# Performance work log

Measured on AMD Instinct MI355X. Metric: run time of the kernel, lower is better.

The kernel has to match this reference:

```python
import jax, jax.numpy as jnp
import numpy as np

B = 50000        # mini-batch nodes
NB, M, D = 4, 256, 32   # branches, codebook size, per-branch dim
C = NB * D       # in_channels = out_channels = 128
E = 1000000      # edges per block (intra and cross)
N_GLOBAL = 100000


def setup_inputs() -> dict:
    key = jax.random.key(0)
    ks = jax.random.split(key, 16)
    return {
        "X_B": jax.random.normal(ks[0], (B, C), dtype=jnp.float32),
        "edge_src_bb": jax.random.randint(ks[1], (E,), 0, B),
        "edge_dst_bb": jax.random.randint(ks[2], (E,), 0, B),
        "edge_w_bb": jax.random.uniform(ks[3], (E,), dtype=jnp.float32),
        "edge_src_bm": jax.random.randint(ks[4], (E,), 0, N_GLOBAL),
        "edge_dst_bm": jax.random.randint(ks[5], (E,), 0, B),
        "edge_w_bm": jax.random.uniform(ks[6], (E,), dtype=jnp.float32),
        "c_indices": jax.random.randint(ks[7], (N_GLOBAL,), 0, M),
        "warm_up_rate": jnp.ones((1,), dtype=jnp.float32),
        "codebook": jax.random.normal(ks[8], (NB, M, D), dtype=jnp.float32),
        "vq_grad": jax.random.normal(ks[9], (NB, M, D), dtype=jnp.float32) * 0.01,
        "W_conv": jax.random.normal(ks[10], (NB, D, D), dtype=jnp.float32) / np.sqrt(D),
        "b_conv": jax.random.normal(ks[11], (NB, D), dtype=jnp.float32) * 0.01,
        "W_fc": jax.random.normal(ks[12], (C, C), dtype=jnp.float32) / np.sqrt(C),
        "b_fc": jax.random.normal(ks[13], (C,), dtype=jnp.float32) * 0.01,
    }


def reference(X_B, edge_src_bb, edge_dst_bb, edge_w_bb, edge_src_bm, edge_dst_bm,
              edge_w_bm, c_indices, warm_up_rate, codebook, vq_grad,
              W_conv, b_conv, W_fc, b_fc):
    wr = warm_up_rate[0]
    # split features into NB branches: [NB, B, D]
    Xb = X_B.reshape(B, NB, D).transpose(1, 0, 2)
    # X_input = cat([X_B, codebook * warm_up_rate]) per branch -> [NB, B+M, D]
    X_in = jnp.concatenate([Xb, codebook * wr], axis=1)
    # GCNConv (normalize=False): linear transform then edge-weighted aggregation
    h = jnp.einsum('nbd,nde->nbe', X_in, W_conv)
    # mapper: remap out-of-batch endpoints of cross edges to codeword rows
    src_bm = B + c_indices[edge_src_bm]          # [E] indices into codeword rows
    out = jnp.zeros_like(h)
    # A_BB block: intra-batch message passing
    out = out.at[:, edge_dst_bb].add(edge_w_bb[None, :, None] * h[:, edge_src_bb])
    # A_BM block: batch nodes receive from codewords (quantized neighbors)
    out = out.at[:, edge_dst_bm].add(edge_w_bm[None, :, None] * h[:, src_bm])
    # A_MB block: codeword rows receive from batch nodes (for info_backward)
    out = out.at[:, src_bm].add(edge_w_bm[None, :, None] * h[:, edge_dst_bm])
    out = out + b_conv[:, None, :]
    # info_backward routes approximated gradient through codeword outputs
    info_backward = jnp.sum(out[:, B:] * vq_grad) * wr
    # concat branch outputs for batch nodes, second fc, skip connection
    Xcat = out[:, :B].transpose(1, 0, 2).reshape(B, C)
    Y = Xcat @ W_fc + b_fc + X_B
    return (Y, info_backward)
```

## Files before the change

kernel.cpp:

```cpp
#include <hip/hip_runtime.h>
#include <hip/hip_bf16.h>

#define BN    50000
#define NBR   4
#define MM    256
#define DD    32
#define CC    128
#define EE    1000000
#define ROWS  (BN + MM)
#define NEDGE (2 * EE)
#define SCAN_BLOCKS 49

template <int ISBF> struct IO;

template <> struct IO<0> {
    static __device__ float ld(const void* p, long i) { return ((const float*)p)[i]; }
    static __device__ float2 ld2(const void* p, long i) {
        const float* f = (const float*)p + i;
        return make_float2(f[0], f[1]);
    }
    static __device__ void st(void* p, long i, float v) { ((float*)p)[i] = v; }
    static __device__ void st2(void* p, long i, float2 v) {
        float* f = (float*)p + i; f[0] = v.x; f[1] = v.y;
    }
};

template <> struct IO<1> {
    static __device__ float b2f(unsigned short u) {
        return __uint_as_float(((unsigned)u) << 16);
    }
    static __device__ unsigned short f2b(float f) {
        unsigned x = __float_as_uint(f);
        unsigned r = x + 0x7fffu + ((x >> 16) & 1u);
        return (unsigned short)(r >> 16);
    }
    static __device__ float ld(const void* p, long i) {
        return b2f(((const unsigned short*)p)[i]);
    }
    static __device__ float2 ld2(const void* p, long i) {
        unsigned v = *(const unsigned*)((const unsigned short*)p + i);
        return make_float2(b2f((unsigned short)(v & 0xffffu)),
                           b2f((unsigned short)(v >> 16)));
    }
    static __device__ void st(void* p, long i, float v) {
        ((unsigned short*)p)[i] = f2b(v);
    }
    static __device__ void st2(void* p, long i, float2 v) {
        unsigned o = ((unsigned)f2b(v.x)) | (((unsigned)f2b(v.y)) << 16);
        *(unsigned*)((unsigned short*)p + i) = o;
    }
};

template <int ISBF> struct HIO;
template <> struct HIO<0> {
    static __device__ float2 ld(const float* h, long row, int l) {
        return *(const float2*)(h + row * CC + 2 * l);
    }
    static __device__ void st(float* h, long row, int l, float2 v) {
        *(float2*)(h + row * CC + 2 * l) = v;
    }
};
template <> struct HIO<1> {
    static __device__ float2 ld(const float* h, long row, int l) {
        unsigned u = ((const unsigned*)h)[row * (CC / 2) + l];
        return make_float2(IO<1>::b2f((unsigned short)(u & 0xffffu)),
                           IO<1>::b2f((unsigned short)(u >> 16)));
    }
    static __device__ void st(float* h, long row, int l, float2 v) {
        unsigned o = ((unsigned)IO<1>::f2b(v.x)) | (((unsigned)IO<1>::f2b(v.y)) << 16);
        ((unsigned*)h)[row * (CC / 2) + l] = o;
    }
};

static __device__ inline void unpack8(int4 v, float* f) {
    unsigned a = (unsigned)v.x, b = (unsigned)v.y, c = (unsigned)v.z, d = (unsigned)v.w;
    f[0] = IO<1>::b2f((unsigned short)(a & 0xffffu)); f[1] = IO<1>::b2f((unsigned short)(a >> 16));
    f[2] = IO<1>::b2f((unsigned short)(b & 0xffffu)); f[3] = IO<1>::b2f((unsigned short)(b >> 16));
    f[4] = IO<1>::b2f((unsigned short)(c & 0xffffu)); f[5] = IO<1>::b2f((unsigned short)(c >> 16));
    f[6] = IO<1>::b2f((unsigned short)(d & 0xffffu)); f[7] = IO<1>::b2f((unsigned short)(d >> 16));
}
static __device__ inline void fma8(float* acc, float w, int4 v) {
    float f[8]; unpack8(v, f);
#pragma unroll
    for (int k = 0; k < 8; k++) acc[k] += w * f[k];
}
static __device__ inline float dot8(const float* hi, int4 v) {
    float f[8]; unpack8(v, f);
    float s = 0.f;
#pragma unroll
    for (int k = 0; k < 8; k++) s += hi[k] * f[k];
    return s;
}

__global__ void kDetect(const void* warm, int* flag) {
    flag[0] = (((const unsigned short*)warm)[0] == 0x3F80u) ? 1 : 0;
}

template <int ISBF>
__device__ void kA_body(const void* X_B, const void* codebook, const void* W_conv,
                        const void* warm, float* __restrict__ hout,
                        float* __restrict__ hcw, float* sW, float* sX) {
    int tid = threadIdx.x;
    int w = tid >> 6, l = tid & 63;
    for (int k = tid; k < NBR * DD * DD; k += 256)
        sW[k] = IO<ISBF>::ld(W_conv, k);
    int r = blockIdx.x * 4 + w;
    int c0 = 2 * l, n = c0 >> 5, e = c0 & 31;
    float2 x2;
    if (r < BN) {
        x2 = IO<ISBF>::ld2(X_B, (long)r * CC + c0);
    } else {
        int m = r - BN;
        float wr = IO<ISBF>::ld(warm, 0);
        x2 = IO<ISBF>::ld2(codebook, (long)n * MM * DD + m * DD + e);
        x2.x *= wr; x2.y *= wr;
    }
    sX[w * CC + c0] = x2.x;
    sX[w * CC + c0 + 1] = x2.y;
    __syncthreads();
    float2 acc = make_float2(0.f, 0.f);
#pragma unroll
    for (int d = 0; d < DD; d++) {
        float xv = sX[w * CC + n * DD + d];
        float2 wv = *(const float2*)&sW[n * DD * DD + d * DD + e];
        acc.x += xv * wv.x;
        acc.y += xv * wv.y;
    }
    if (r < BN) HIO<ISBF>::st(hout, r, l, acc);
    else        HIO<ISBF>::st(hcw, r - BN, l, acc);
}
__global__ __launch_bounds__(256) void kA(const int* flag, const void* X_B,
                                          const void* codebook, const void* W_conv,
                                          const void* warm, float* hout, float* hcw) {
    __shared__ float sW[NBR * DD * DD];
    __shared__ float sX[4 * CC];
    if (*flag) kA_body<1>(X_B, codebook, W_conv, warm, hout, hcw, sW, sX);
    else       kA_body<0>(X_B, codebook, W_conv, warm, hout, hcw, sW, sX);
}

__global__ void kHist(const int* __restrict__ edst_bb, const int* __restrict__ edst_bm,
                      int* __restrict__ counts) {
    long stride = (long)gridDim.x * blockDim.x;
    for (long i = (long)blockIdx.x * blockDim.x + threadIdx.x; i < NEDGE; i += stride) {
        int dst = (i < EE) ? edst_bb[i] : edst_bm[i - EE];
        atomicAdd(&counts[dst], 1);
    }
}

__global__ __launch_bounds__(1024) void kScan1(const int* __restrict__ counts,
                                               int* __restrict__ offsets,
                                               int* __restrict__ tileSum) {
    __shared__ int s[1024];
    int tid = threadIdx.x;
    int i = blockIdx.x * 1024 + tid;
    int v = (i < BN) ? counts[i] : 0;
    s[tid] = v;
    __syncthreads();
    for (int off = 1; off < 1024; off <<= 1) {
        int x = (tid >= off) ? s[tid - off] : 0;
        __syncthreads();
        s[tid] += x;
        __syncthreads();
    }
    if (i < BN) offsets[i] = s[tid] - v;
    if (tid == 1023) tileSum[blockIdx.x] = s[tid];
}
__global__ void kScan2(int* tileSum) {
    int run = 0;
    for (int t = 0; t < SCAN_BLOCKS; t++) {
        int v = tileSum[t];
        tileSum[t] = run;
        run += v;
    }
}
__global__ __launch_bounds__(1024) void kScan3(int* __restrict__ offsets,
                                               const int* __restrict__ tileSum,
                                               int* __restrict__ cursor) {
    int i = blockIdx.x * 1024 + threadIdx.x;
    if (i < BN) {
        int o = offsets[i] + tileSum[blockIdx.x];
        offsets[i] = o;
        cursor[i] = o;
    }
}

template <int ISBF>
__device__ void kFill_body(const int* esrc_bb, const int* edst_bb, const void* ew_bb,
                           const int* esrc_bm, const int* edst_bm, const void* ew_bm,
                           const int* c_idx, int* cursor, int2* entries) {
    long stride = (long)gridDim.x * blockDim.x;
    for (long i = (long)blockIdx.x * blockDim.x + threadIdx.x; i < NEDGE; i += stride) {
        int src, dst; float w;
        if (i < EE) {
            src = esrc_bb[i]; dst = edst_bb[i]; w = IO<ISBF>::ld(ew_bb, i);
        } else {
            long j = i - EE;
            src = BN + c_idx[esrc_bm[j]]; dst = edst_bm[j]; w = IO<ISBF>::ld(ew_bm, j);
        }
        int pos = atomicAdd(&cursor[dst], 1);
        entries[pos] = make_int2(src, __float_as_int(w));
    }
}
__global__ void kFill(const int* flag, const int* esrc_bb, const int* edst_bb,
                      const void* ew_bb, const int* esrc_bm, const int* edst_bm,
                      const void* ew_bm, const int* c_idx, int* cursor, int2* entries) {
    if (*flag) kFill_body<1>(esrc_bb, edst_bb, ew_bb, esrc_bm, edst_bm, ew_bm, c_idx, cursor, entries);
    else       kFill_body<0>(esrc_bb, edst_bb, ew_bb, esrc_bm, edst_bm, ew_bm, c_idx, cursor, entries);
}

__device__ void kG_body_bf(const unsigned short* __restrict__ hbatch,
                           const unsigned short* __restrict__ hcw,
                           const int2* __restrict__ entries,
                           const int* __restrict__ offsets, const int* __restrict__ counts,
                           const void* b_conv, const void* vq_grad, void* t,
                           float* __restrict__ infoP, int4* sCW) {
    int tid = threadIdx.x;
    const int4* cwsrc = (const int4*)hcw;
    for (int k = tid; k < MM * CC * 2 / 16; k += 1024) sCW[k] = cwsrc[k];
    __syncthreads();
    const char* sB = (const char*)sCW;

    int w = tid >> 6, l = tid & 63;
    int i = blockIdx.x * 16 + w;
    int g = l >> 4;
    int q = l & 15;
    int c0 = q * 8;
    int n = c0 >> 5, e0 = c0 & 31;
    int start = __builtin_amdgcn_readfirstlane(offsets[i]);
    int deg   = __builtin_amdgcn_readfirstlane(counts[i]);
    const int2* ep = entries + start;
    const unsigned short* gb = (const unsigned short*)vq_grad + (long)n * MM * DD + e0;

    float hi[8];
    unpack8(*(const int4*)(hbatch + (long)i * CC + c0), hi);
    float acc[8] = {0.f, 0.f, 0.f, 0.f, 0.f, 0.f, 0.f, 0.f};
    float info = 0.f;

    int j = 0;
    for (; j + 32 <= deg; j += 32) {
        int2 ev[8];
#pragma unroll
        for (int u = 0; u < 8; u++) ev[u] = ep[j + 4 * u + g];
#pragma unroll
        for (int u = 0; u < 8; u++) {
            float wj = __int_as_float(ev[u].y);
            int4 hv;
            if (ev[u].x < BN) {
                hv = *(const int4*)(hbatch + (long)ev[u].x * CC + c0);
            } else {
                hv = *(const int4*)(sB + (((long)(ev[u].x - BN)) << 8) + (q << 4));
                int4 gv = *(const int4*)(gb + (long)(ev[u].x - BN) * DD);
                info += wj * dot8(hi, gv);
            }
            fma8(acc, wj, hv);
        }
    }
    for (; j < deg; j += 4) {
        int idx = j + g;
        int2 ev = ep[idx < deg ? idx : j];
        float wj = (idx < deg) ? __int_as_float(ev.y) : 0.f;
        int4 hv;
        if (ev.x < BN) {
            hv = *(const int4*)(hbatch + (long)ev.x * CC + c0);
        } else {
            hv = *(const int4*)(sB + (((long)(ev.x - BN)) << 8) + (q << 4));
            if (wj != 0.f) {
                int4 gv = *(const int4*)(gb + (long)(ev.x - BN) * DD);
                info += wj * dot8(hi, gv);
            }
        }
        fma8(acc, wj, hv);
    }
#pragma unroll
    for (int k = 0; k < 8; k++) {
        acc[k] += __shfl_xor(acc[k], 16);
        acc[k] += __shfl_xor(acc[k], 32);
    }
    for (int off = 32; off; off >>= 1) info += __shfl_xor(info, off);
    if (l == 0) infoP[i] = info;
    if (g == 0) {
        float bc[8];
        unpack8(*(const int4*)((const unsigned short*)b_conv + n * DD + e0), bc);
        unsigned o[4];
#pragma unroll
        for (int d = 0; d < 4; d++)
            o[d] = ((unsigned)IO<1>::f2b(acc[2 * d] + bc[2 * d])) |
                   (((unsigned)IO<1>::f2b(acc[2 * d + 1] + bc[2 * d + 1])) << 16);
        *(int4*)((unsigned short*)t + (long)i * CC + c0) = make_int4(o[0], o[1], o[2], o[3]);
    }
}

__device__ void kG_body_f32(const float* __restrict__ hbatch, const float* __restrict__ hcw,
                            const int2* __restrict__ entries,
                            const int* __restrict__ offsets, const int* __restrict__ counts,
                            const void* b_conv, const void* vq_grad, void* t,
                            float* __restrict__ infoP) {
    int tid = threadIdx.x;
    int w = tid >> 6, l = tid & 63;
    int i = blockIdx.x * 16 + w;
    int c0 = 2 * l, n = c0 >> 5, e = c0 & 31;
    int start = __builtin_amdgcn_readfirstlane(offsets[i]);
    int deg   = __builtin_amdgcn_readfirstlane(counts[i]);
    const int2* ep = entries + start;
    float2 hi = HIO<0>::ld(hbatch, i, l);
    long gbase = (long)n * MM * DD + e;
    float2 acc = make_float2(0.f, 0.f);
    float info = 0.f;
    for (int j = 0; j < deg; j++) {
        int2 ev = ep[j];
        float wj = __int_as_float(ev.y);
        const float* src = (ev.x < BN) ? (hbatch + (long)ev.x * CC)
                                       : (hcw + (long)(ev.x - BN) * CC);
        float2 hv = *(const float2*)(src + c0);
        acc.x += wj * hv.x;
        acc.y += wj * hv.y;
        if (ev.x >= BN) {
            float2 gv = IO<0>::ld2(vq_grad, gbase + (long)(ev.x - BN) * DD);
            info += wj * (hi.x * gv.x + hi.y * gv.y);
        }
    }
    float2 b2 = IO<0>::ld2(b_conv, n * DD + e);
    IO<0>::st2(t, (long)i * CC + c0, make_float2(acc.x + b2.x, acc.y + b2.y));
    for (int off = 32; off; off >>= 1) info += __shfl_xor(info, off);
    if (l == 0) infoP[i] = info;
}
__global__ __launch_bounds__(1024, 8) void kGather(const int* flag, const float* hout,
                                                   const float* hcw, const int2* entries,
                                                   const int* offsets, const int* counts,
                                                   const void* b_conv, const void* vq_grad,
                                                   void* t, float* infoP) {
    __shared__ int4 sCW[MM * CC * 2 / 16];
    if (*flag) kG_body_bf((const unsigned short*)hout, (const unsigned short*)hcw,
                          entries, offsets, counts, b_conv, vq_grad, t, infoP, sCW);
    else       kG_body_f32(hout, hcw, entries, offsets, counts, b_conv, vq_grad, t, infoP);
}

__global__ __launch_bounds__(1024) void kRed(const float* __restrict__ infoP, float* ibAcc) {
    __shared__ float s[1024];
    int tid = threadIdx.x;
    int i = blockIdx.x * 1024 + tid;
    s[tid] = (i < BN) ? infoP[i] : 0.f;
    __syncthreads();
    for (int st = 512; st; st >>= 1) {
        if (tid < st) s[tid] += s[tid + st];
        __syncthreads();
    }
    if (tid == 0) atomicAdd(ibAcc, s[0]);
}

template <int ISBF>
__device__ void kFC_body(const void* t, const void* W_fc, const void* b_fc,
                         const void* X_B, void* Y, float* sT, float* sW) {
    int tid = threadIdx.x;
    int w = tid >> 6, l = tid & 63;
    int c0 = 2 * l;
    int r0 = blockIdx.x * 32;
    for (int k = tid; k < 32 * CC / 2; k += 512) {
        int row = k >> 6, c = (k & 63) * 2;
        float2 v = make_float2(0.f, 0.f);
        if (r0 + row < BN) v = IO<ISBF>::ld2(t, (long)(r0 + row) * CC + c);
        sT[row * CC + c] = v.x;
        sT[row * CC + c + 1] = v.y;
    }
    float2 y[4];
#pragma unroll
    for (int rr = 0; rr < 4; rr++) y[rr] = make_float2(0.f, 0.f);
    for (int ch = 0; ch < 4; ch++) {
        __syncthreads();
        for (int k = tid; k < 32 * CC / 2; k += 512) {
            int cc = k >> 6, c = (k & 63) * 2;
            float2 v = IO<ISBF>::ld2(W_fc, (long)(ch * 32 + cc) * CC + c);
            sW[cc * CC + c] = v.x;
            sW[cc * CC + c + 1] = v.y;
        }
        __syncthreads();
#pragma unroll 8
        for (int cc = 0; cc < 32; cc++) {
            float2 wv = *(const float2*)&sW[cc * CC + c0];
#pragma unroll
            for (int rr = 0; rr < 4; rr++) {
                float tv = sT[(w * 4 + rr) * CC + ch * 32 + cc];
                y[rr].x += tv * wv.x;
                y[rr].y += tv * wv.y;
            }
        }
    }
    float2 bf = IO<ISBF>::ld2(b_fc, c0);
#pragma unroll
    for (int rr = 0; rr < 4; rr++) {
        int r = r0 + w * 4 + rr;
        if (r < BN) {
            float2 xb = IO<ISBF>::ld2(X_B, (long)r * CC + c0);
            IO<ISBF>::st2(Y, (long)r * CC + c0,
                          make_float2(y[rr].x + bf.x + xb.x, y[rr].y + bf.y + xb.y));
        }
    }
}
__global__ __launch_bounds__(512) void kFC(const int* flag, const void* t, const void* W_fc,
                                           const void* b_fc, const void* X_B, void* Y) {
    __shared__ float sT[32 * CC];
    __shared__ float sW[32 * CC];
    if (*flag) kFC_body<1>(t, W_fc, b_fc, X_B, Y, sT, sW);
    else       kFC_body<0>(t, W_fc, b_fc, X_B, Y, sT, sW);
}

template <int ISBF>
__device__ void kF_body(const void* b_conv, const void* vq_grad, const void* warm,
                        const float* ibAcc, void* out, float* sred) {
    int tid = threadIdx.x;
    float a = 0.f;
    for (int idx = tid; idx < NBR * MM * DD; idx += 256) {
        int nn = idx >> 13, dd = idx & 31;
        a += IO<ISBF>::ld(b_conv, nn * DD + dd) * IO<ISBF>::ld(vq_grad, idx);
    }
    sred[tid] = a;
    __syncthreads();
    for (int s = 128; s; s >>= 1) {
        if (tid < s) sred[tid] += sred[tid + s];
        __syncthreads();
    }
    if (tid == 0) {
        float wr = IO<ISBF>::ld(warm, 0);
        IO<ISBF>::st(out, (long)BN * CC, wr * (ibAcc[0] + sred[0]));
    }
}
__global__ __launch_bounds__(256) void kFinal(const int* flag, const void* b_conv,
                                              const void* vq_grad, const void* warm,
                                              const float* ibAcc, void* out) {
    __shared__ float sred[256];
    if (*flag) kF_body<1>(b_conv, vq_grad, warm, ibAcc, out, sred);
    else       kF_body<0>(b_conv, vq_grad, warm, ibAcc, out, sred);
}

extern "C" void kernel_launch(void* const* d_in, const int* in_sizes, int n_in,
                              void* d_out, int out_size, void* d_ws, size_t ws_size,
                              hipStream_t stream) {
    (void)in_sizes; (void)n_in; (void)out_size;
    const void* X_B      = d_in[0];
    const int*  esrc_bb  = (const int*)d_in[1];
    const int*  edst_bb  = (const int*)d_in[2];
    const void* ew_bb    = d_in[3];
    const int*  esrc_bm  = (const int*)d_in[4];
    const int*  edst_bm  = (const int*)d_in[5];
    const void* ew_bm    = d_in[6];
    const int*  c_idx    = (const int*)d_in[7];
    const void* warm     = d_in[8];
    const void* codebook = d_in[9];
    const void* vq_grad  = d_in[10];
    const void* W_conv   = d_in[11];
    const void* b_conv   = d_in[12];
    const void* W_fc     = d_in[13];
    const void* b_fc     = d_in[14];

    char* ws = (char*)d_ws;
    float* hcw     = (float*)ws;  ws += (size_t)MM * CC * 4;
    float* tbuf    = (float*)ws;  ws += (size_t)BN * CC * 4;
    int2*  entries = (int2*)ws;   ws += (size_t)NEDGE * 8;
    int*   counts  = (int*)ws;    ws += (size_t)BN * 4;
    int*   offsets = (int*)ws;    ws += (size_t)BN * 4;
    int*   cursor  = (int*)ws;    ws += (size_t)BN * 4;
    float* infoP   = (float*)ws;  ws += (size_t)BN * 4;
    int*   tileSum = (int*)ws;    ws += 64 * 4;
    float* ibAcc   = (float*)ws;  ws += 16;
    int*   flag    = (int*)ws;    ws += 16;
    if ((size_t)(ws - (char*)d_ws) > ws_size) return;

    float* hout = (float*)d_out;

    hipMemsetAsync(counts, 0, (size_t)BN * 4, stream);
    hipMemsetAsync(ibAcc, 0, 4, stream);
    kDetect<<<1, 1, 0, stream>>>(warm, flag);
    kA<<<ROWS / 4, 256, 0, stream>>>(flag, X_B, codebook, W_conv, warm, hout, hcw);
    kHist<<<1024, 256, 0, stream>>>(edst_bb, edst_bm, counts);
    kScan1<<<SCAN_BLOCKS, 1024, 0, stream>>>(counts, offsets, tileSum);
    kScan2<<<1, 1, 0, stream>>>(tileSum);
    kScan3<<<SCAN_BLOCKS, 1024, 0, stream>>>(offsets, tileSum, cursor);
    kFill<<<1024, 256, 0, stream>>>(flag, esrc_bb, edst_bb, ew_bb, esrc_bm, edst_bm,
                                    ew_bm, c_idx, cursor, entries);
    kGather<<<BN / 16, 1024, 0, stream>>>(flag, hout, hcw, entries, offsets, counts,
                                          b_conv, vq_grad, tbuf, infoP);
    kRed<<<SCAN_BLOCKS, 1024, 0, stream>>>(infoP, ibAcc);
    kFC<<<(BN + 31) / 32, 512, 0, stream>>>(flag, tbuf, W_fc, b_fc, X_B, d_out);
    kFinal<<<1, 256, 0, stream>>>(flag, b_conv, vq_grad, warm, ibAcc, d_out);
}
```

Before: 659.1 us.

## Use persistent grid-stride gather and drop shared-memory codebook staging

The gather kernel becomes persistent: 2048 blocks of 256 threads, with each wavefront striding over destination rows, instead of one 1024-thread block per 16 rows. The per-block copy of the codeword features into shared memory, and the barrier after it, are removed. Codeword rows are now read from global memory and are expected to stay in cache. The main loop and the tail loop are merged into one clamped, masked loop. This cuts the repeated 64KB LDS staging and the launch overhead, but codeword reads now go through L2/L1 instead of LDS.

```diff
diff --git a/kernel.cpp b/kernel.cpp
--- a/kernel.cpp
+++ b/kernel.cpp
@@ -213,80 +213,70 @@
                            const int2* __restrict__ entries,
                            const int* __restrict__ offsets, const int* __restrict__ counts,
                            const void* b_conv, const void* vq_grad, void* t,
-                           float* __restrict__ infoP, int4* sCW) {
-    int tid = threadIdx.x;
-    const int4* cwsrc = (const int4*)hcw;
-    for (int k = tid; k < MM * CC * 2 / 16; k += 1024) sCW[k] = cwsrc[k];
-    __syncthreads();
-    const char* sB = (const char*)sCW;
-
-    int w = tid >> 6, l = tid & 63;
-    int i = blockIdx.x * 16 + w;
+                           float* __restrict__ infoP) {
+    int tid = threadIdx.x;
+    int l = tid & 63;
     int g = l >> 4;
     int q = l & 15;
     int c0 = q * 8;
     int n = c0 >> 5, e0 = c0 & 31;
-    int start = __builtin_amdgcn_readfirstlane(offsets[i]);
-    int deg   = __builtin_amdgcn_readfirstlane(counts[i]);
-    const int2* ep = entries + start;
     const unsigned short* gb = (const unsigned short*)vq_grad + (long)n * MM * DD + e0;
 
-    float hi[8];
-    unpack8(*(const int4*)(hbatch + (long)i * CC + c0), hi);
-    float acc[8] = {0.f, 0.f, 0.f, 0.f, 0.f, 0.f, 0.f, 0.f};
-    float info = 0.f;
-
-    int j = 0;
-    for (; j + 32 <= deg; j += 32) {
-        int2 ev[8];
-#pragma unroll
-        for (int u = 0; u < 8; u++) ev[u] = ep[j + 4 * u + g];
-#pragma unroll
-        for (int u = 0; u < 8; u++) {
-            float wj = __int_as_float(ev[u].y);
-            int4 hv;
-            if (ev[u].x < BN) {
-                hv = *(const int4*)(hbatch + (long)ev[u].x * CC + c0);
-            } else {
-                hv = *(const int4*)(sB + (((long)(ev[u].x - BN)) << 8) + (q << 4));
-                int4 gv = *(const int4*)(gb + (long)(ev[u].x - BN) * DD);
-                info += wj * dot8(hi, gv);
+    int wid = (int)((blockIdx.x * blockDim.x + tid) >> 6);
+    int nw  = (int)((gridDim.x * blockDim.x) >> 6);
+
+    for (int i = wid; i < BN; i += nw) {
+        int start = __builtin_amdgcn_readfirstlane(offsets[i]);
+        int deg   = __builtin_amdgcn_readfirstlane(counts[i]);
+        const int2* ep = entries + start;
+
+        float hi[8];
+        unpack8(*(const int4*)(hbatch + (long)i * CC + c0), hi);
+        float acc[8] = {0.f, 0.f, 0.f, 0.f, 0.f, 0.f, 0.f, 0.f};
+        float info = 0.f;
+
+        for (int j = 0; j < deg; j += 32) {
+            int2 ev[8];
+            float wj[8];
+#pragma unroll
+            for (int u = 0; u < 8; u++) {
+                int idx = j + 4 * u + g;
+                int cl = idx < deg ? idx : deg - 1;
+                ev[u] = ep[cl];
+                wj[u] = (idx < deg) ? __int_as_float(ev[u].y) : 0.f;
             }
-            fma8(acc, wj, hv);
-        }
-    }
-    for (; j < deg; j += 4) {
-        int idx = j + g;
-        int2 ev = ep[idx < deg ? idx : j];
-        float wj = (idx < deg) ? __int_as_float(ev.y) : 0.f;
-        int4 hv;
-        if (ev.x < BN) {
-            hv = *(const int4*)(hbatch + (long)ev.x * CC + c0);
-        } else {
-            hv = *(const int4*)(sB + (((long)(ev.x - BN)) << 8) + (q << 4));
-            if (wj != 0.f) {
-                int4 gv = *(const int4*)(gb + (long)(ev.x - BN) * DD);
-                info += wj * dot8(hi, gv);
+#pragma unroll
+            for (int u = 0; u < 8; u++) {
+                int4 hv;
+                if (ev[u].x < BN) {
+                    hv = *(const int4*)(hbatch + (long)ev[u].x * CC + c0);
+                } else {
+                    hv = *(const int4*)(hcw + (long)(ev[u].x - BN) * CC + c0);
+                    if (wj[u] != 0.f) {
+                        int4 gv = *(const int4*)(gb + (long)(ev[u].x - BN) * DD);
+                        info += wj[u] * dot8(hi, gv);
+                    }
+                }
+                fma8(acc, wj[u], hv);
             }
         }
-        fma8(acc, wj, hv);
-    }
-#pragma unroll
-    for (int k = 0; k < 8; k++) {
-        acc[k] += __shfl_xor(acc[k], 16);
-        acc[k] += __shfl_xor(acc[k], 32);
-    }
-    for (int off = 32; off; off >>= 1) info += __shfl_xor(info, off);
-    if (l == 0) infoP[i] = info;
-    if (g == 0) {
-        float bc[8];
-        unpack8(*(const int4*)((const unsigned short*)b_conv + n * DD + e0), bc);
-        unsigned o[4];
-#pragma unroll
-        for (int d = 0; d < 4; d++)
-            o[d] = ((unsigned)IO<1>::f2b(acc[2 * d] + bc[2 * d])) |
-                   (((unsigned)IO<1>::f2b(acc[2 * d + 1] + bc[2 * d + 1])) << 16);
-        *(int4*)((unsigned short*)t + (long)i * CC + c0) = make_int4(o[0], o[1], o[2], o[3]);
+#pragma unroll
+        for (int k = 0; k < 8; k++) {
+            acc[k] += __shfl_xor(acc[k], 16);
+            acc[k] += __shfl_xor(acc[k], 32);
+        }
+        for (int off = 32; off; off >>= 1) info += __shfl_xor(info, off);
+        if (l == 0) infoP[i] = info;
+        if (g == 0) {
+            float bc[8];
+            unpack8(*(const int4*)((const unsigned short*)b_conv + n * DD + e0), bc);
+            unsigned o[4];
+#pragma unroll
+            for (int d = 0; d < 4; d++)
+                o[d] = ((unsigned)IO<1>::f2b(acc[2 * d] + bc[2 * d])) |
+                       (((unsigned)IO<1>::f2b(acc[2 * d + 1] + bc[2 * d + 1])) << 16);
+            *(int4*)((unsigned short*)t + (long)i * CC + c0) = make_int4(o[0], o[1], o[2], o[3]);
+        }
     }
 }
 
@@ -296,42 +286,44 @@
                             const void* b_conv, const void* vq_grad, void* t,
                             float* __restrict__ infoP) {
     int tid = threadIdx.x;
-    int w = tid >> 6, l = tid & 63;
-    int i = blockIdx.x * 16 + w;
+    int l = tid & 63;
     int c0 = 2 * l, n = c0 >> 5, e = c0 & 31;
-    int start = __builtin_amdgcn_readfirstlane(offsets[i]);
-    int deg   = __builtin_amdgcn_readfirstlane(counts[i]);
-    const int2* ep = entries + start;
-    float2 hi = HIO<0>::ld(hbatch, i, l);
-    long gbase = (long)n * MM * DD + e;
-    float2 acc = make_float2(0.f, 0.f);
-    float info = 0.f;
-    for (int j = 0; j < deg; j++) {
-        int2 ev = ep[j];
-        float wj = __int_as_float(ev.y);
-        const float* src = (ev.x < BN) ? (hbatch + (long)ev.x * CC)
-                                       : (hcw + (long)(ev.x - BN) * CC);
-        float2 hv = *(const float2*)(src + c0);
-        acc.x += wj * hv.x;
-        acc.y += wj * hv.y;
-        if (ev.x >= BN) {
-            float2 gv = IO<0>::ld2(vq_grad, gbase + (long)(ev.x - BN) * DD);
-            info += wj * (hi.x * gv.x + hi.y * gv.y);
-        }
-    }
-    float2 b2 = IO<0>::ld2(b_conv, n * DD + e);
-    IO<0>::st2(t, (long)i * CC + c0, make_float2(acc.x + b2.x, acc.y + b2.y));
-    for (int off = 32; off; off >>= 1) info += __shfl_xor(info, off);
-    if (l == 0) infoP[i] = info;
-}
-__global__ __launch_bounds__(1024, 8) void kGather(const int* flag, const float* hout,
-                                                   const float* hcw, const int2* entries,
-                                                   const int* offsets, const int* counts,
-                                                   const void* b_conv, const void* vq_grad,
-                                                   void* t, float* infoP) {
-    __shared__ int4 sCW[MM * CC * 2 / 16];
+    int wid = (int)((blockIdx.x * blockDim.x + tid) >> 6);
+    int nw  = (int)((gridDim.x * blockDim.x) >> 6);
+    for (int i = wid; i < BN; i += nw) {
+        int start = __builtin_amdgcn_readfirstlane(offsets[i]);
+        int deg   = __builtin_amdgcn_readfirstlane(counts[i]);
+        const int2* ep = entries + start;
+        float2 hi = HIO<0>::ld(hbatch, i, l);
+        long gbase = (long)n * MM * DD + e;
+        float2 acc = make_float2(0.f, 0.f);
+        float info = 0.f;
+        for (int j = 0; j < deg; j++) {
+            int2 ev = ep[j];
+            float wj = __int_as_float(ev.y);
+            const float* src = (ev.x < BN) ? (hbatch + (long)ev.x * CC)
+                                           : (hcw + (long)(ev.x - BN) * CC);
+            float2 hv = *(const float2*)(src + c0);
+            acc.x += wj * hv.x;
+            acc.y += wj * hv.y;
+            if (ev.x >= BN) {
+                float2 gv = IO<0>::ld2(vq_grad, gbase + (long)(ev.x - BN) * DD);
+                info += wj * (hi.x * gv.x + hi.y * gv.y);
+            }
+        }
+        float2 b2 = IO<0>::ld2(b_conv, n * DD + e);
+        IO<0>::st2(t, (long)i * CC + c0, make_float2(acc.x + b2.x, acc.y + b2.y));
+        for (int off = 32; off; off >>= 1) info += __shfl_xor(info, off);
+        if (l == 0) infoP[i] = info;
+    }
+}
+__global__ __launch_bounds__(256, 8) void kGather(const int* flag, const float* hout,
+                                                  const float* hcw, const int2* entries,
+                                                  const int* offsets, const int* counts,
+                                                  const void* b_conv, const void* vq_grad,
+                                                  void* t, float* infoP) {
     if (*flag) kG_body_bf((const unsigned short*)hout, (const unsigned short*)hcw,
-                          entries, offsets, counts, b_conv, vq_grad, t, infoP, sCW);
+                          entries, offsets, counts, b_conv, vq_grad, t, infoP);
     else       kG_body_f32(hout, hcw, entries, offsets, counts, b_conv, vq_grad, t, infoP);
 }
 
@@ -477,8 +469,8 @@
     kScan3<<<SCAN_BLOCKS, 1024, 0, stream>>>(offsets, tileSum, cursor);
     kFill<<<1024, 256, 0, stream>>>(flag, esrc_bb, edst_bb, ew_bb, esrc_bm, edst_bm,
                                     ew_bm, c_idx, cursor, entries);
-    kGather<<<BN / 16, 1024, 0, stream>>>(flag, hout, hcw, entries, offsets, counts,
-                                          b_conv, vq_grad, tbuf, infoP);
+    kGather<<<2048, 256, 0, stream>>>(flag, hout, hcw, entries, offsets, counts,
+                                      b_conv, vq_grad, tbuf, infoP);
     kRed<<<SCAN_BLOCKS, 1024, 0, stream>>>(infoP, ibAcc);
     kFC<<<(BN + 31) / 32, 512, 0, stream>>>(flag, tbuf, W_fc, b_fc, X_B, d_out);
     kFinal<<<1, 256, 0, stream>>>(flag, b_conv, vq_grad, warm, ibAcc, d_out);
```

New measurement: 636.9 us. 1.03x faster.
